# Optimization experiments

Measured on AMD Instinct MI355X. Metric: run time of the kernel, lower is better.

Reference implementation:

```python
import jax, jax.numpy as jnp
import numpy as np

HEADS = 16
DIM_HEAD = 64
LN_EPS = 1e-5
COS_EPS = 1e-8


def setup_inputs() -> dict:
    key = jax.random.key(0)
    ks = jax.random.split(key, 5)
    dim = 1024
    inner = HEADS * DIM_HEAD
    q = jax.random.normal(ks[0], (4, 1024, dim), dtype=jnp.float32)
    k = jax.random.normal(ks[1], (4, 2048, dim), dtype=jnp.float32)
    v = jax.random.normal(ks[2], (4, 2048, dim), dtype=jnp.float32)
    W_in = jax.random.normal(ks[3], (dim, inner), dtype=jnp.float32) * (1.0 / np.sqrt(dim))
    W_out = jax.random.normal(ks[4], (inner, dim), dtype=jnp.float32) * (1.0 / np.sqrt(inner))
    ln_gamma = jnp.ones((dim,), dtype=jnp.float32)
    ln_beta = jnp.zeros((dim,), dtype=jnp.float32)
    b_out = jnp.zeros((dim,), dtype=jnp.float32)
    return {"q": q, "k": k, "v": v, "ln_gamma": ln_gamma, "ln_beta": ln_beta,
            "W_in": W_in, "W_out": W_out, "b_out": b_out}


def _layernorm(x, gamma, beta):
    mu = jnp.mean(x, axis=-1, keepdims=True)
    var = jnp.mean(jnp.square(x - mu), axis=-1, keepdims=True)  # biased, as torch
    return (x - mu) * jax.lax.rsqrt(var + LN_EPS) * gamma + beta


def _project(t, gamma, beta, W_in):
    # LayerNorm -> Linear(no bias) -> split heads: b n (h d) -> b h n d
    x = _layernorm(t, gamma, beta) @ W_in
    b, n, _ = x.shape
    return x.reshape(b, n, HEADS, DIM_HEAD).transpose(0, 2, 1, 3)


def reference(q, k, v, ln_gamma, ln_beta, W_in, W_out, b_out):
    f_q = _project(q, ln_gamma, ln_beta, W_in)  # [b,h,n,d]
    f_k = _project(k, ln_gamma, ln_beta, W_in)  # [b,h,m,d]
    f_v = _project(v, ln_gamma, ln_beta, W_in)  # [b,h,m,d]
    dots = jnp.einsum('bhnd,bhmd->bhnm', f_q, f_k)
    qn = jnp.linalg.norm(f_q, axis=-1, keepdims=True)          # [b,h,n,1]
    kn = jnp.linalg.norm(f_k, axis=-1, keepdims=True)          # [b,h,m,1]
    attn = dots / (qn * kn.transpose(0, 1, 3, 2) + COS_EPS)    # [b,h,n,m]
    out = jnp.einsum('bhnm,bhmd->bhnd', attn, f_v)             # [b,h,n,d]
    b, h, n, d = out.shape
    out = out.transpose(0, 2, 1, 3).reshape(b, n, h * d)       # b n (h d)
    return out @ W_out + b_out
```

## Files before the change

### kernel.cpp

```cpp
#include <hip/hip_runtime.h>

constexpr int BATCH = 4;
constexpr int SEQQ  = 1024;
constexpr int SEQK  = 2048;
constexpr int DIM   = 1024;
constexpr int NH    = 16;
constexpr int DH    = 64;
constexpr int RQ    = BATCH * SEQQ;
constexpr int RK    = BATCH * SEQK;
constexpr int RTOT  = RQ + 2 * RK;
constexpr int BH    = BATCH * NH;
constexpr int NSLC  = 8;
constexpr float LN_EPS = 1e-5f;

typedef _Float16 f16;
typedef __attribute__((ext_vector_type(8))) _Float16 f16x8;
typedef __attribute__((ext_vector_type(4))) float f32x4;

__device__ __forceinline__ void async16(const void* g, void* l) {
  __builtin_amdgcn_global_load_lds(
      (const __attribute__((address_space(1))) void*)g,
      (__attribute__((address_space(3))) void*)l, 16, 0, 0);
}

__global__ void __launch_bounds__(256) prep_kernel(
    const float* __restrict__ q, const float* __restrict__ k,
    const float* __restrict__ v, const float* __restrict__ gamma,
    const float* __restrict__ beta, f16* __restrict__ a_h,
    const float* __restrict__ W0, const float* __restrict__ W1,
    f16* __restrict__ T0, f16* __restrict__ T1) {
  __shared__ float tile[32][33];
  if (blockIdx.x < RTOT / 4) {
    const int row = blockIdx.x * 4 + (threadIdx.x >> 6);
    const int lane = threadIdx.x & 63;
    const float* src;
    if (row < RQ)            src = q + (size_t)row * DIM;
    else if (row < RQ + RK)  src = k + (size_t)(row - RQ) * DIM;
    else                     src = v + (size_t)(row - RQ - RK) * DIM;
    float4 x[4];
    float s = 0.f, s2 = 0.f;
#pragma unroll
    for (int c = 0; c < 4; c++) {
      x[c] = ((const float4*)src)[c * 64 + lane];
      s  += x[c].x + x[c].y + x[c].z + x[c].w;
      s2 += x[c].x * x[c].x + x[c].y * x[c].y + x[c].z * x[c].z + x[c].w * x[c].w;
    }
#pragma unroll
    for (int off = 1; off < 64; off <<= 1) {
      s  += __shfl_xor(s, off);
      s2 += __shfl_xor(s2, off);
    }
    const float mu = s / DIM;
    const float rs = rsqrtf(s2 / DIM - mu * mu + LN_EPS);
#pragma unroll
    for (int c = 0; c < 4; c++) {
      float4 g = ((const float4*)gamma)[c * 64 + lane];
      float4 b = ((const float4*)beta)[c * 64 + lane];
      union { f16 h[4]; uint2 u; } o;
      o.h[0] = (f16)((x[c].x - mu) * rs * g.x + b.x);
      o.h[1] = (f16)((x[c].y - mu) * rs * g.y + b.y);
      o.h[2] = (f16)((x[c].z - mu) * rs * g.z + b.z);
      o.h[3] = (f16)((x[c].w - mu) * rs * g.w + b.w);
      ((uint2*)(a_h + (size_t)row * DIM))[c * 64 + lane] = o.u;
    }
  } else {
    const int bid = blockIdx.x - RTOT / 4;
    const int z = bid >> 10;
    const int rem = bid & 1023;
    const float* W = z ? W1 : W0;
    f16* T = z ? T1 : T0;
    const int k0 = (rem >> 5) * 32, n0 = (rem & 31) * 32;
    const int tx = threadIdx.x & 31, ty = threadIdx.x >> 5;
#pragma unroll
    for (int i = 0; i < 4; i++)
      tile[ty + 8 * i][tx] = W[(size_t)(k0 + ty + 8 * i) * DIM + n0 + tx];
    __syncthreads();
#pragma unroll
    for (int i = 0; i < 4; i++)
      T[(size_t)(n0 + ty + 8 * i) * DIM + k0 + tx] = (f16)tile[tx][ty + 8 * i];
  }
}

template <int MT, bool OUT_F16, bool NORMS, bool BIAS, bool PERB>
__global__ void __launch_bounds__(256) mfma_gemm(
    const f16* __restrict__ A, const f16* __restrict__ Bt,
    void* __restrict__ Cout, const float* __restrict__ bias) {
  constexpr int JT = (MT == 128) ? 4 : 2;
  __shared__ f16 As[2][MT * 32];
  __shared__ f16 Bs[2][128 * 32];
  const int t = threadIdx.x;
  const int wid = t >> 6;
  const int lane = t & 63;
  const int row0 = blockIdx.x * MT;
  const int col0 = blockIdx.y * 128;
  const int wm = (MT == 128) ? (wid >> 1) * 64 : 0;
  const int wn = (MT == 128) ? (wid & 1) * 64 : wid * 32;

  const f16* BtB = PERB ? Bt + (size_t)(row0 >> 10) * DIM * DIM : Bt;

  const int rB = 32 * wid + (lane >> 2);
  const int qB = ((lane & 3) - ((rB >> 1) & 3)) & 3;
  const f16* gB = BtB + (size_t)(col0 + rB) * DIM + qB * 8;
  f16* lB0 = Bs[0] + 32 * wid * 32;
  f16* lB1 = Bs[1] + 32 * wid * 32;
  const int rA = (MT == 128 ? 32 : 16) * wid + (lane >> 2);
  const int qA = ((lane & 3) - ((rA >> 1) & 3)) & 3;
  const f16* gA = A + (size_t)(row0 + rA) * DIM + qA * 8;
  f16* lA0 = As[0] + (MT == 128 ? 32 : 16) * wid * 32;
  f16* lA1 = As[1] + (MT == 128 ? 32 : 16) * wid * 32;

  f32x4 acc[4][JT];
#pragma unroll
  for (int i = 0; i < 4; i++)
#pragma unroll
    for (int j = 0; j < JT; j++) acc[i][j] = (f32x4){0.f, 0.f, 0.f, 0.f};

  const int mrow = lane & 15;
  const int kq_p = (((lane >> 4) + ((lane >> 1) & 3)) & 3) * 8;

  for (int kt = 0; kt < DIM / 64; ++kt) {
    if (kt) __syncthreads();
    const int ko = kt * 64;
    async16(gA + ko,      lA0);
    if (MT == 128) async16(gA + ko + 16 * DIM, lA0 + 512);
    async16(gB + ko,      lB0);
    async16(gB + ko + 16 * DIM, lB0 + 512);
    async16(gA + ko + 32, lA1);
    if (MT == 128) async16(gA + ko + 32 + 16 * DIM, lA1 + 512);
    async16(gB + ko + 32, lB1);
    async16(gB + ko + 32 + 16 * DIM, lB1 + 512);
    __syncthreads();

#pragma unroll
    for (int h = 0; h < 2; ++h) {
      f16x8 af[4], bf[JT];
#pragma unroll
      for (int i = 0; i < 4; i++)
        af[i] = *(const f16x8*)(As[h] + (wm + i * 16 + mrow) * 32 + kq_p);
#pragma unroll
      for (int j = 0; j < JT; j++)
        bf[j] = *(const f16x8*)(Bs[h] + (wn + j * 16 + mrow) * 32 + kq_p);
#pragma unroll
      for (int i = 0; i < 4; i++)
#pragma unroll
        for (int j = 0; j < JT; j++)
          acc[i][j] = __builtin_amdgcn_mfma_f32_16x16x32_f16(af[i], bf[j], acc[i][j], 0, 0, 0);
    }
  }

  if (NORMS && MT == 128) {
    if (row0 < RQ + RK) {
      float sums[4][4];
#pragma unroll
      for (int i = 0; i < 4; i++)
#pragma unroll
        for (int r = 0; r < 4; r++) {
          float s = 0.f;
#pragma unroll
          for (int j = 0; j < JT; j++) s += acc[i][j][r] * acc[i][j][r];
          sums[i][r] = s;
        }
#pragma unroll
      for (int off = 1; off < 16; off <<= 1)
#pragma unroll
        for (int i = 0; i < 4; i++)
#pragma unroll
          for (int r = 0; r < 4; r++)
            sums[i][r] += __shfl_xor(sums[i][r], off);
#pragma unroll
      for (int i = 0; i < 4; i++)
#pragma unroll
        for (int r = 0; r < 4; r++) {
          const float inv = rsqrtf(sums[i][r]);
#pragma unroll
          for (int j = 0; j < JT; j++) acc[i][j][r] *= inv;
        }
    }
  }

  const int ccol = lane & 15;
  const int crow = (lane >> 4) * 4;
  if (OUT_F16) {
    f16* C = (f16*)Cout;
#pragma unroll
    for (int j = 0; j < JT; j++) {
      const int col = col0 + wn + j * 16 + ccol;
#pragma unroll
      for (int i = 0; i < 4; i++) {
        f16* Cp = C + (size_t)(row0 + wm + i * 16 + crow) * DIM + col;
#pragma unroll
        for (int r = 0; r < 4; r++) Cp[(size_t)r * DIM] = (f16)acc[i][j][r];
      }
    }
  } else {
    float* C = (float*)Cout;
#pragma unroll
    for (int j = 0; j < JT; j++) {
      const int col = col0 + wn + j * 16 + ccol;
      float bv = BIAS ? bias[col] : 0.f;
#pragma unroll
      for (int i = 0; i < 4; i++) {
        float* Cp = C + (size_t)(row0 + wm + i * 16 + crow) * DIM + col;
#pragma unroll
        for (int r = 0; r < 4; r++) Cp[(size_t)r * DIM] = acc[i][j][r] + bv;
      }
    }
  }
}

__global__ void __launch_bounds__(256) s_kernel(
    const f16* __restrict__ f, float* __restrict__ S4) {
  const int bh = blockIdx.x;
  const int b = bh >> 4, h = bh & 15;
  const int wid = threadIdx.x >> 6, lane = threadIdx.x & 63;
  const int m0 = blockIdx.y * (SEQK / NSLC) + wid * 64;
  const int d1 = (lane & 7) * 8;
  const int d2 = ((lane >> 3) & 7) * 8;
  const f16* kb = f + ((size_t)RQ + (size_t)b * SEQK + m0) * DIM + h * DH + d1;
  const f16* vb = f + ((size_t)RQ + RK + (size_t)b * SEQK + m0) * DIM + h * DH + d2;

  float acc[8][8];
#pragma unroll
  for (int i = 0; i < 8; i++)
#pragma unroll
    for (int j = 0; j < 8; j++) acc[i][j] = 0.f;

#pragma unroll 4
  for (int m = 0; m < 64; ++m) {
    f16x8 kf = *(const f16x8*)(kb + (size_t)m * DIM);
    f16x8 vf = *(const f16x8*)(vb + (size_t)m * DIM);
    float kx[8], vx[8];
#pragma unroll
    for (int e = 0; e < 8; e++) { kx[e] = (float)kf[e]; vx[e] = (float)vf[e]; }
#pragma unroll
    for (int i = 0; i < 8; i++)
#pragma unroll
      for (int j = 0; j < 8; j++)
        acc[i][j] = fmaf(kx[i], vx[j], acc[i][j]);
  }

  __shared__ float Sacc[4][64][68];
#pragma unroll
  for (int i = 0; i < 8; i++) {
    *(float4*)&Sacc[wid][d1 + i][d2]     = *(float4*)&acc[i][0];
    *(float4*)&Sacc[wid][d1 + i][d2 + 4] = *(float4*)&acc[i][4];
  }
  __syncthreads();
  const int t = threadIdx.x;
  const int r = t >> 2, c0 = (t & 3) * 16;
  float* Sp = S4 + ((size_t)blockIdx.y * BH + bh) * (DH * DH) + r * DH + c0;
#pragma unroll
  for (int c4 = 0; c4 < 4; c4++) {
    float4 s = {0.f, 0.f, 0.f, 0.f};
#pragma unroll
    for (int w = 0; w < 4; w++) {
      float4 p = *(const float4*)&Sacc[w][r][c0 + 4 * c4];
      s.x += p.x; s.y += p.y; s.z += p.z; s.w += p.w;
    }
    *(float4*)(Sp + 4 * c4) = s;
  }
}

__global__ void __launch_bounds__(256) s_reduce(
    const float* __restrict__ S4, f16* __restrict__ Sh) {
  const int bh = blockIdx.x;
  const int t = threadIdx.x;
  const size_t base = (size_t)bh * DH * DH + t * 16;
  constexpr size_t STR = (size_t)BH * DH * DH;
#pragma unroll
  for (int c = 0; c < 4; c++) {
    float4 s = {0.f, 0.f, 0.f, 0.f};
#pragma unroll
    for (int p = 0; p < NSLC; p++) {
      float4 sp = *(const float4*)(S4 + base + p * STR + 4 * c);
      s.x += sp.x; s.y += sp.y; s.z += sp.z; s.w += sp.w;
    }
    union { f16 h[4]; uint2 u; } o;
    o.h[0] = (f16)s.x; o.h[1] = (f16)s.y; o.h[2] = (f16)s.z; o.h[3] = (f16)s.w;
    *(uint2*)(Sh + base + 4 * c) = o.u;
  }
}

__global__ void __launch_bounds__(256) m_build(
    const f16* __restrict__ wt_out, const f16* __restrict__ Sh,
    f16* __restrict__ Mt) {
  const int n0 = blockIdx.x * 128;
  const int bh = blockIdx.y;
  const int b = bh >> 4, h = bh & 15;
  __shared__ f16 As[128 * 64];
  __shared__ f16 Bs[64 * 64];
  const int t = threadIdx.x;
  const int wid = t >> 6, lane = t & 63;

  const f16* gA = wt_out + (size_t)(n0 + 32 * wid + (lane >> 3)) * DIM
                  + 64 * h + (lane & 7) * 8;
  f16* lA = As + 32 * wid * 64;
  const f16* gB = Sh + (size_t)bh * DH * DH + (16 * wid + (lane >> 3)) * 64
                  + (lane & 7) * 8;
  f16* lB = Bs + 16 * wid * 64;
#pragma unroll
  for (int o = 0; o < 4; o++) async16(gA + (size_t)(8 * o) * DIM, lA + 8 * o * 64);
  async16(gB, lB);
  async16(gB + 8 * 64, lB + 8 * 64);
  __syncthreads();

  const int wm = (wid >> 1) * 64;
  const int wn = (wid & 1) * 32;
  const int mrow = lane & 15;
  f32x4 acc[4][2];
#pragma unroll
  for (int i = 0; i < 4; i++)
#pragma unroll
    for (int j = 0; j < 2; j++) acc[i][j] = (f32x4){0.f, 0.f, 0.f, 0.f};

#pragma unroll
  for (int kh = 0; kh < 2; kh++) {
    const int kq = kh * 32 + (lane >> 4) * 8;
    f16x8 af[4], bf[2];
#pragma unroll
    for (int i = 0; i < 4; i++)
      af[i] = *(const f16x8*)(As + (wm + i * 16 + mrow) * 64 + kq);
#pragma unroll
    for (int j = 0; j < 2; j++)
      bf[j] = *(const f16x8*)(Bs + (wn + j * 16 + mrow) * 64 + kq);
#pragma unroll
    for (int i = 0; i < 4; i++)
#pragma unroll
      for (int j = 0; j < 2; j++)
        acc[i][j] = __builtin_amdgcn_mfma_f32_16x16x32_f16(af[i], bf[j], acc[i][j], 0, 0, 0);
  }

  const int ccol = lane & 15;
  const int crow = (lane >> 4) * 4;
  f16* Mb = Mt + (size_t)b * DIM * DIM;
#pragma unroll
  for (int j = 0; j < 2; j++) {
    const int col = 64 * h + wn + j * 16 + ccol;
#pragma unroll
    for (int i = 0; i < 4; i++) {
      f16* Mp = Mb + (size_t)(n0 + wm + i * 16 + crow) * DIM + col;
#pragma unroll
      for (int r = 0; r < 4; r++) Mp[(size_t)r * DIM] = (f16)acc[i][j][r];
    }
  }
}

extern "C" void kernel_launch(void* const* d_in, const int* in_sizes, int n_in,
                              void* d_out, int out_size, void* d_ws, size_t ws_size,
                              hipStream_t stream) {
  const float* q     = (const float*)d_in[0];
  const float* k     = (const float*)d_in[1];
  const float* v     = (const float*)d_in[2];
  const float* gamma = (const float*)d_in[3];
  const float* beta  = (const float*)d_in[4];
  const float* W_in  = (const float*)d_in[5];
  const float* W_out = (const float*)d_in[6];
  const float* b_out = (const float*)d_in[7];
  float* out = (float*)d_out;

  char* w = (char*)d_ws;
  f16*   f      = (f16*)w;
  f16*   a_h    = f + (size_t)RTOT * DIM;
  f16*   wt_in  = a_h + (size_t)RTOT * DIM;
  f16*   wt_out = wt_in + (size_t)DIM * DIM;
  f16*   Mt     = wt_out + (size_t)DIM * DIM;
  f16*   Sh     = Mt + (size_t)BATCH * DIM * DIM;
  float* S4     = (float*)(Sh + (size_t)BH * DH * DH);

  prep_kernel<<<RTOT / 4 + 2048, 256, 0, stream>>>(
      q, k, v, gamma, beta, a_h, W_in, W_out, wt_in, wt_out);

  mfma_gemm<128, true, true, false, false>
      <<<dim3(RTOT / 128, DIM / 128), 256, 0, stream>>>(a_h, wt_in, f, nullptr);

  s_kernel<<<dim3(BH, NSLC), 256, 0, stream>>>(f, S4);

  s_reduce<<<BH, 256, 0, stream>>>(S4, Sh);

  m_build<<<dim3(DIM / 128, BH), 256, 0, stream>>>(wt_out, Sh, Mt);

  mfma_gemm<64, false, false, true, true>
      <<<dim3(RQ / 64, DIM / 128), 256, 0, stream>>>(f, Mt, out, b_out);
}
```

Before: 242.4 us.

## Fuse slice reduction into m_build and use 64x64 tiles for output GEMM

Removes the separate s_reduce kernel: m_build now sums the eight per-slice S partials in fp32 and writes the fp16 result straight into shared memory, saving a launch and a global round trip. The final output GEMM switches from 64x128 to 64x64 tiles, doubling the block count to 1024 for better CU occupancy at the cost of more redundant A loads. The S4 scratch buffer now aliases the a_h region, which is dead after the projection GEMM.

```diff
diff --git a/kernel.cpp b/kernel.cpp
--- a/kernel.cpp
+++ b/kernel.cpp
@@ -81,37 +81,41 @@
   }
 }
 
-template <int MT, bool OUT_F16, bool NORMS, bool BIAS, bool PERB>
+template <int MT, int NT, bool OUT_F16, bool NORMS, bool BIAS, bool PERB>
 __global__ void __launch_bounds__(256) mfma_gemm(
     const f16* __restrict__ A, const f16* __restrict__ Bt,
     void* __restrict__ Cout, const float* __restrict__ bias) {
+  constexpr int IT = (MT == 128) ? 4 : (NT == 128 ? 4 : 2);
   constexpr int JT = (MT == 128) ? 4 : 2;
+  constexpr int AR = (MT == 128) ? 32 : 16;
+  constexpr int BR = (NT == 128) ? 32 : 16;
   __shared__ f16 As[2][MT * 32];
-  __shared__ f16 Bs[2][128 * 32];
+  __shared__ f16 Bs[2][NT * 32];
   const int t = threadIdx.x;
   const int wid = t >> 6;
   const int lane = t & 63;
   const int row0 = blockIdx.x * MT;
-  const int col0 = blockIdx.y * 128;
-  const int wm = (MT == 128) ? (wid >> 1) * 64 : 0;
-  const int wn = (MT == 128) ? (wid & 1) * 64 : wid * 32;
+  const int col0 = blockIdx.y * NT;
+  const int wm = (MT == 128) ? (wid >> 1) * 64 : (NT == 128 ? 0 : (wid >> 1) * 32);
+  const int wn = (MT == 128) ? (wid & 1) * 64
+                             : (NT == 128 ? wid * 32 : (wid & 1) * 32);
 
   const f16* BtB = PERB ? Bt + (size_t)(row0 >> 10) * DIM * DIM : Bt;
 
-  const int rB = 32 * wid + (lane >> 2);
+  const int rB = BR * wid + (lane >> 2);
   const int qB = ((lane & 3) - ((rB >> 1) & 3)) & 3;
   const f16* gB = BtB + (size_t)(col0 + rB) * DIM + qB * 8;
-  f16* lB0 = Bs[0] + 32 * wid * 32;
-  f16* lB1 = Bs[1] + 32 * wid * 32;
-  const int rA = (MT == 128 ? 32 : 16) * wid + (lane >> 2);
+  f16* lB0 = Bs[0] + BR * wid * 32;
+  f16* lB1 = Bs[1] + BR * wid * 32;
+  const int rA = AR * wid + (lane >> 2);
   const int qA = ((lane & 3) - ((rA >> 1) & 3)) & 3;
   const f16* gA = A + (size_t)(row0 + rA) * DIM + qA * 8;
-  f16* lA0 = As[0] + (MT == 128 ? 32 : 16) * wid * 32;
-  f16* lA1 = As[1] + (MT == 128 ? 32 : 16) * wid * 32;
-
-  f32x4 acc[4][JT];
-#pragma unroll
-  for (int i = 0; i < 4; i++)
+  f16* lA0 = As[0] + AR * wid * 32;
+  f16* lA1 = As[1] + AR * wid * 32;
+
+  f32x4 acc[IT][JT];
+#pragma unroll
+  for (int i = 0; i < IT; i++)
 #pragma unroll
     for (int j = 0; j < JT; j++) acc[i][j] = (f32x4){0.f, 0.f, 0.f, 0.f};
 
@@ -124,35 +128,35 @@
     async16(gA + ko,      lA0);
     if (MT == 128) async16(gA + ko + 16 * DIM, lA0 + 512);
     async16(gB + ko,      lB0);
-    async16(gB + ko + 16 * DIM, lB0 + 512);
+    if (NT == 128) async16(gB + ko + 16 * DIM, lB0 + 512);
     async16(gA + ko + 32, lA1);
     if (MT == 128) async16(gA + ko + 32 + 16 * DIM, lA1 + 512);
     async16(gB + ko + 32, lB1);
-    async16(gB + ko + 32 + 16 * DIM, lB1 + 512);
+    if (NT == 128) async16(gB + ko + 32 + 16 * DIM, lB1 + 512);
     __syncthreads();
 
 #pragma unroll
     for (int h = 0; h < 2; ++h) {
-      f16x8 af[4], bf[JT];
-#pragma unroll
-      for (int i = 0; i < 4; i++)
+      f16x8 af[IT], bf[JT];
+#pragma unroll
+      for (int i = 0; i < IT; i++)
         af[i] = *(const f16x8*)(As[h] + (wm + i * 16 + mrow) * 32 + kq_p);
 #pragma unroll
       for (int j = 0; j < JT; j++)
         bf[j] = *(const f16x8*)(Bs[h] + (wn + j * 16 + mrow) * 32 + kq_p);
 #pragma unroll
-      for (int i = 0; i < 4; i++)
+      for (int i = 0; i < IT; i++)
 #pragma unroll
         for (int j = 0; j < JT; j++)
           acc[i][j] = __builtin_amdgcn_mfma_f32_16x16x32_f16(af[i], bf[j], acc[i][j], 0, 0, 0);
     }
   }
 
-  if (NORMS && MT == 128) {
+  if (NORMS && MT == 128 && NT == 128) {
     if (row0 < RQ + RK) {
-      float sums[4][4];
-#pragma unroll
-      for (int i = 0; i < 4; i++)
+      float sums[IT][4];
+#pragma unroll
+      for (int i = 0; i < IT; i++)
 #pragma unroll
         for (int r = 0; r < 4; r++) {
           float s = 0.f;
@@ -163,12 +167,12 @@
 #pragma unroll
       for (int off = 1; off < 16; off <<= 1)
 #pragma unroll
-        for (int i = 0; i < 4; i++)
+        for (int i = 0; i < IT; i++)
 #pragma unroll
           for (int r = 0; r < 4; r++)
             sums[i][r] += __shfl_xor(sums[i][r], off);
 #pragma unroll
-      for (int i = 0; i < 4; i++)
+      for (int i = 0; i < IT; i++)
 #pragma unroll
         for (int r = 0; r < 4; r++) {
           const float inv = rsqrtf(sums[i][r]);
@@ -186,7 +190,7 @@
     for (int j = 0; j < JT; j++) {
       const int col = col0 + wn + j * 16 + ccol;
 #pragma unroll
-      for (int i = 0; i < 4; i++) {
+      for (int i = 0; i < IT; i++) {
         f16* Cp = C + (size_t)(row0 + wm + i * 16 + crow) * DIM + col;
 #pragma unroll
         for (int r = 0; r < 4; r++) Cp[(size_t)r * DIM] = (f16)acc[i][j][r];
@@ -199,7 +203,7 @@
       const int col = col0 + wn + j * 16 + ccol;
       float bv = BIAS ? bias[col] : 0.f;
 #pragma unroll
-      for (int i = 0; i < 4; i++) {
+      for (int i = 0; i < IT; i++) {
         float* Cp = C + (size_t)(row0 + wm + i * 16 + crow) * DIM + col;
 #pragma unroll
         for (int r = 0; r < 4; r++) Cp[(size_t)r * DIM] = acc[i][j][r] + bv;
@@ -261,28 +265,8 @@
   }
 }
 
-__global__ void __launch_bounds__(256) s_reduce(
-    const float* __restrict__ S4, f16* __restrict__ Sh) {
-  const int bh = blockIdx.x;
-  const int t = threadIdx.x;
-  const size_t base = (size_t)bh * DH * DH + t * 16;
-  constexpr size_t STR = (size_t)BH * DH * DH;
-#pragma unroll
-  for (int c = 0; c < 4; c++) {
-    float4 s = {0.f, 0.f, 0.f, 0.f};
-#pragma unroll
-    for (int p = 0; p < NSLC; p++) {
-      float4 sp = *(const float4*)(S4 + base + p * STR + 4 * c);
-      s.x += sp.x; s.y += sp.y; s.z += sp.z; s.w += sp.w;
-    }
-    union { f16 h[4]; uint2 u; } o;
-    o.h[0] = (f16)s.x; o.h[1] = (f16)s.y; o.h[2] = (f16)s.z; o.h[3] = (f16)s.w;
-    *(uint2*)(Sh + base + 4 * c) = o.u;
-  }
-}
-
 __global__ void __launch_bounds__(256) m_build(
-    const f16* __restrict__ wt_out, const f16* __restrict__ Sh,
+    const f16* __restrict__ wt_out, const float* __restrict__ S4,
     f16* __restrict__ Mt) {
   const int n0 = blockIdx.x * 128;
   const int bh = blockIdx.y;
@@ -295,13 +279,27 @@
   const f16* gA = wt_out + (size_t)(n0 + 32 * wid + (lane >> 3)) * DIM
                   + 64 * h + (lane & 7) * 8;
   f16* lA = As + 32 * wid * 64;
-  const f16* gB = Sh + (size_t)bh * DH * DH + (16 * wid + (lane >> 3)) * 64
-                  + (lane & 7) * 8;
-  f16* lB = Bs + 16 * wid * 64;
 #pragma unroll
   for (int o = 0; o < 4; o++) async16(gA + (size_t)(8 * o) * DIM, lA + 8 * o * 64);
-  async16(gB, lB);
-  async16(gB + 8 * 64, lB + 8 * 64);
+
+  {
+    const size_t base = (size_t)bh * (DH * DH) + t * 16;
+    constexpr size_t STR = (size_t)BH * DH * DH;
+    union { f16 h16[16]; f16x8 v8[2]; } hv;
+#pragma unroll
+    for (int c = 0; c < 4; c++) {
+      float4 s = {0.f, 0.f, 0.f, 0.f};
+#pragma unroll
+      for (int p = 0; p < NSLC; p++) {
+        float4 sp = *(const float4*)(S4 + base + p * STR + 4 * c);
+        s.x += sp.x; s.y += sp.y; s.z += sp.z; s.w += sp.w;
+      }
+      hv.h16[4 * c + 0] = (f16)s.x; hv.h16[4 * c + 1] = (f16)s.y;
+      hv.h16[4 * c + 2] = (f16)s.z; hv.h16[4 * c + 3] = (f16)s.w;
+    }
+    *(f16x8*)(Bs + t * 16)     = hv.v8[0];
+    *(f16x8*)(Bs + t * 16 + 8) = hv.v8[1];
+  }
   __syncthreads();
 
   const int wm = (wid >> 1) * 64;
@@ -364,21 +362,18 @@
   f16*   wt_in  = a_h + (size_t)RTOT * DIM;
   f16*   wt_out = wt_in + (size_t)DIM * DIM;
   f16*   Mt     = wt_out + (size_t)DIM * DIM;
-  f16*   Sh     = Mt + (size_t)BATCH * DIM * DIM;
-  float* S4     = (float*)(Sh + (size_t)BH * DH * DH);
+  float* S4     = (float*)a_h;
 
   prep_kernel<<<RTOT / 4 + 2048, 256, 0, stream>>>(
       q, k, v, gamma, beta, a_h, W_in, W_out, wt_in, wt_out);
 
-  mfma_gemm<128, true, true, false, false>
+  mfma_gemm<128, 128, true, true, false, false>
       <<<dim3(RTOT / 128, DIM / 128), 256, 0, stream>>>(a_h, wt_in, f, nullptr);
 
   s_kernel<<<dim3(BH, NSLC), 256, 0, stream>>>(f, S4);
 
-  s_reduce<<<BH, 256, 0, stream>>>(S4, Sh);
-
-  m_build<<<dim3(DIM / 128, BH), 256, 0, stream>>>(wt_out, Sh, Mt);
-
-  mfma_gemm<64, false, false, true, true>
-      <<<dim3(RQ / 64, DIM / 128), 256, 0, stream>>>(f, Mt, out, b_out);
-}
+  m_build<<<dim3(DIM / 128, BH), 256, 0, stream>>>(wt_out, S4, Mt);
+
+  mfma_gemm<64, 64, false, false, true, true>
+      <<<dim3(RQ / 64, DIM / 64), 256, 0, stream>>>(f, Mt, out, b_out);
+}
```

Result: slower. 254.7 us (+5.1%).
